# Performance work log

Hardware: AMD Instinct MI355X
Metric: run time of the kernel (lower is better)

Reference implementation:

```python
import jax, jax.numpy as jnp
import numpy as np

B, C, H, W = 8, 384, 32, 32
NUM_HEADS = 8
HEAD_DIM = C // NUM_HEADS
HIDDEN = max(32, C // 2)


def setup_inputs() -> dict:
    key = jax.random.key(0)
    ks = jax.random.split(key, 6)
    s = lambda fan_in: 1.0 / np.sqrt(fan_in)
    return {
        "x": jax.random.normal(ks[0], (B, C, H, W), dtype=jnp.float32),
        "qkv_w": jax.random.normal(ks[1], (C, 3 * C), dtype=jnp.float32) * s(C),
        "qkv_b": jnp.zeros((3 * C,), dtype=jnp.float32),
        "proj_w": jax.random.normal(ks[2], (C, C), dtype=jnp.float32) * s(C),
        "proj_b": jnp.zeros((C,), dtype=jnp.float32),
        "mlp_w1": jax.random.normal(ks[3], (2, HIDDEN), dtype=jnp.float32) * s(2),
        "mlp_b1": jnp.zeros((HIDDEN,), dtype=jnp.float32),
        "mlp_w2": jax.random.normal(ks[4], (HIDDEN, NUM_HEADS), dtype=jnp.float32) * s(HIDDEN),
        "mlp_b2": jnp.zeros((NUM_HEADS,), dtype=jnp.float32),
    }


def _relative_bias(h, w, mlp_w1, mlp_b1, mlp_w2, mlp_b2):
    ch = jnp.arange(h, dtype=jnp.float32)
    cw = jnp.arange(w, dtype=jnp.float32)
    coords = jnp.stack(jnp.meshgrid(ch, cw, indexing="ij"), axis=-1).reshape(-1, 2)  # [N,2]
    rel = coords[:, None, :] - coords[None, :, :]  # [N,N,2]
    denom = jnp.array([max(h - 1, 1), max(w - 1, 1)], dtype=jnp.float32)
    rel = rel / denom
    hidden = jax.nn.gelu(rel @ mlp_w1 + mlp_b1, approximate=False)
    bias = hidden @ mlp_w2 + mlp_b2  # [N,N,heads]
    return jnp.transpose(bias, (2, 0, 1))  # [heads,N,N]


def reference(x, qkv_w, qkv_b, proj_w, proj_b, mlp_w1, mlp_b1, mlp_w2, mlp_b2):
    b, c, h, w = x.shape
    n = h * w
    tokens = x.reshape(b, c, n).transpose(0, 2, 1)  # [B,N,C]
    qkv = (tokens @ qkv_w + qkv_b).reshape(b, n, 3, NUM_HEADS, HEAD_DIM)
    qkv = jnp.transpose(qkv, (2, 0, 3, 1, 4))  # [3,B,h,N,d]
    q, k, v = qkv[0], qkv[1], qkv[2]
    scale = HEAD_DIM ** -0.5
    attn = jnp.einsum("bhnd,bhmd->bhnm", q * scale, k)
    attn = attn + _relative_bias(h, w, mlp_w1, mlp_b1, mlp_w2, mlp_b2)[None]
    attn = jax.nn.softmax(attn, axis=-1)
    out = jnp.einsum("bhnm,bhmd->bhnd", attn, v)
    out = out.transpose(0, 2, 1, 3).reshape(b, n, c)
    out = out @ proj_w + proj_b
    return out.transpose(0, 2, 1).reshape(b, c, h, w)
```

## Files before the change

### kernel.cpp

```cpp
#include <hip/hip_runtime.h>
#include <hip/hip_bf16.h>
#include <math.h>

#define BB 8
#define CC 384
#define NT 1024
#define NHEAD 8
#define HD 48
#define HIDDEN 192
#define THREEC 1152

typedef short short8 __attribute__((ext_vector_type(8)));
typedef short short4v __attribute__((ext_vector_type(4)));
typedef float f32x4 __attribute__((ext_vector_type(4)));
typedef unsigned int uint2v __attribute__((ext_vector_type(2)));

static __device__ __forceinline__ short bf16bits(float v) {
  __hip_bfloat16 h = __float2bfloat16(v);
  return *(short*)&h;
}
static __device__ __forceinline__ unsigned pk2(float a, float b) {
  return __builtin_amdgcn_perm(__float_as_uint(b) + 0x8000u,
                               __float_as_uint(a) + 0x8000u, 0x07060302u);
}
static __device__ __forceinline__ void lds_dma16(const void* g, void* l) {
  __builtin_amdgcn_global_load_lds((const __attribute__((address_space(1))) unsigned*)g,
                                   (__attribute__((address_space(3))) unsigned*)l, 16, 0, 0);
}

__global__ __launch_bounds__(256) void k_prep(
    const float* __restrict__ x, const float* __restrict__ qkv_w,
    const float* __restrict__ proj_w,
    const float* __restrict__ w1, const float* __restrict__ b1,
    const float* __restrict__ w2, const float* __restrict__ b2,
    __hip_bfloat16* __restrict__ xt, __hip_bfloat16* __restrict__ wtq,
    __hip_bfloat16* __restrict__ wtp, float* __restrict__ tab) {
  const int bid = blockIdx.x;
  const int tid = threadIdx.x;
  if (bid >= 3648) {
    int g = (bid - 3648) * 256 + tid;
    int p = g >> 3, jc = g & 7;
    if (p >= 63 * 63) return;
    float rh = (float)(p / 63 - 31) * (1.0f / 31.0f);
    float rw = (float)(p % 63 - 31) * (1.0f / 31.0f);
    float acc[8] = {0.f, 0.f, 0.f, 0.f, 0.f, 0.f, 0.f, 0.f};
    const int j0 = jc * 24;
#pragma unroll 4
    for (int j = j0; j < j0 + 24; j++) {
      float pre = fmaf(rh, w1[j], fmaf(rw, w1[HIDDEN + j], b1[j]));
      float gl = 0.5f * pre * (1.0f + erff(pre * 0.70710678118654752f));
#pragma unroll
      for (int h = 0; h < 8; h++) acc[h] = fmaf(gl, w2[j * 8 + h], acc[h]);
    }
#pragma unroll
    for (int msk = 1; msk <= 4; msk <<= 1)
#pragma unroll
      for (int h = 0; h < 8; h++) acc[h] += __shfl_xor(acc[h], msk);
    if (jc == 0) {
#pragma unroll
      for (int h = 0; h < 8; h++)
        tab[h * 3969 + p] = (acc[h] + b2[h]) * 1.4426950408889634f;
    }
    return;
  }
  const float* src;
  __hip_bfloat16* dst;
  int R, C, r0, c0;
  if (bid < 3072) {
    int zi = bid / 384, rem = bid % 384;
    R = 384; C = 1024;
    r0 = (rem / 32) * 32; c0 = (rem % 32) * 32;
    src = x + (size_t)zi * R * C;
    dst = xt + (size_t)zi * R * C;
  } else if (bid < 3504) {
    int i = bid - 3072;
    R = 384; C = 1152;
    r0 = (i / 36) * 32; c0 = (i % 36) * 32;
    src = qkv_w; dst = wtq;
  } else {
    int i = bid - 3504;
    R = 384; C = 384;
    r0 = (i / 12) * 32; c0 = (i % 12) * 32;
    src = proj_w; dst = wtp;
  }
  __shared__ float t[32][33];
#pragma unroll
  for (int e = 0; e < 4; e++) {
    int i = tid + e * 256;
    int r = i >> 5, c = i & 31;
    t[r][c] = src[(size_t)(r0 + r) * C + c0 + c];
  }
  __syncthreads();
#pragma unroll
  for (int e = 0; e < 4; e++) {
    int i = tid + e * 256;
    int c = i >> 5, r = i & 31;
    dst[(size_t)(c0 + c) * R + r0 + r] = __float2bfloat16(t[r][c]);
  }
}

__global__ __launch_bounds__(256) void k_qkv_mfma(
    const __hip_bfloat16* __restrict__ xt,
    const __hip_bfloat16* __restrict__ wtq,
    const float* __restrict__ qkv_b,
    __hip_bfloat16* __restrict__ Qb,
    __hip_bfloat16* __restrict__ Kb,
    __hip_bfloat16* __restrict__ Vt)
{
  __shared__ __align__(16) char smem[17408];
  short* As = (short*)smem;
  short* Bs = (short*)(smem + 8192);
  float* Vf = (float*)smem;
  const int n0 = blockIdx.x * 64;
  const int m0 = blockIdx.y * 64;
  const int tid = threadIdx.x;
  const int wv = tid >> 6, lane = tid & 63, quad = lane >> 4, lq = lane & 15;
  const int lrow = lane >> 3;
  const int gsw = ((lane & 7) ^ lrow) * 8;
  const int sw0 = (quad ^ (lq & 7)) * 8;
  const int sw1 = sw0 ^ 32;
  f32x4 acc[4];
#pragma unroll
  for (int nt = 0; nt < 4; nt++) acc[nt] = (f32x4){0.f, 0.f, 0.f, 0.f};
  for (int kk = 0; kk < CC; kk += 64) {
    __syncthreads();
    for (int c = wv; c < 16; c += 4) {
      if (c < 8)
        lds_dma16((const short*)xt + (size_t)(m0 + c * 8 + lrow) * 384 + kk + gsw,
                  smem + c * 1024);
      else
        lds_dma16((const short*)wtq + (size_t)(n0 + (c - 8) * 8 + lrow) * 384 + kk + gsw,
                  smem + 8192 + (c - 8) * 1024);
    }
    __syncthreads();
    short8 a0 = *(const short8*)(As + (wv * 16 + lq) * 64 + sw0);
    short8 a1 = *(const short8*)(As + (wv * 16 + lq) * 64 + sw1);
#pragma unroll
    for (int nt = 0; nt < 4; nt++) {
      acc[nt] = __builtin_amdgcn_mfma_f32_16x16x32_bf16(
          a0, *(const short8*)(Bs + (nt * 16 + lq) * 64 + sw0), acc[nt], 0, 0, 0);
      acc[nt] = __builtin_amdgcn_mfma_f32_16x16x32_bf16(
          a1, *(const short8*)(Bs + (nt * 16 + lq) * 64 + sw1), acc[nt], 0, 0, 0);
    }
  }
  __syncthreads();
  const float qscale = 0.14433756729740643f * 1.4426950408889634f;
  const float sc = (n0 < 384) ? qscale : 1.0f;
#pragma unroll
  for (int nt = 0; nt < 4; nt++) {
    float bias = qkv_b[n0 + nt * 16 + lq];
#pragma unroll
    for (int r = 0; r < 4; r++)
      Vf[(nt * 16 + lq) * 68 + wv * 16 + quad * 4 + r] = (acc[nt][r] + bias) * sc;
  }
  __syncthreads();
  if (n0 >= 768) {
    int ch = tid & 63, grp = tid >> 6;
    int cg = n0 - 768 + ch;
    int head = cg / 48, d = cg - head * 48;
    int b = m0 >> 10;
    int n = (m0 & 1023) + grp * 16;
    const float* src = Vf + ch * 68 + grp * 16;
    short o16[16];
#pragma unroll
    for (int k = 0; k < 16; k++) o16[k] = bf16bits(src[k]);
    short* dst = (short*)Vt + ((size_t)(b * 8 + head) * 48 + d) * 1024 + n;
    *(short8*)dst = *(short8*)o16;
    *(short8*)(dst + 8) = *(short8*)(o16 + 8);
  } else {
    const int which = n0 >= 384;
    short* Out = which ? (short*)Kb : (short*)Qb;
    int n_l = tid & 63, seg = tid >> 6;
    int rr0 = (n0 - which * 384) + seg * 16;
    int head = rr0 / 48, d0 = rr0 - head * 48;
    int b = m0 >> 10;
    int n_g = (m0 & 1023) + n_l;
    const float* src = Vf + (seg * 16) * 68 + n_l;
    short o16[16];
#pragma unroll
    for (int k = 0; k < 16; k++) o16[k] = bf16bits(src[k * 68]);
    short* dst = Out + (((size_t)(b * 8 + head) << 10) + n_g) * 64 + d0;
    *(short8*)dst = *(short8*)o16;
    *(short8*)(dst + 8) = *(short8*)(o16 + 8);
    if (d0 == 0) {
      short8 z = (short8){0, 0, 0, 0, 0, 0, 0, 0};
      *(short8*)(dst + 48) = z;
      *(short8*)(dst + 56) = z;
    }
  }
}

#define K0_OFF 0
#define K1_OFF 8192
#define V0_OFF 16384
#define V1_OFF 22528
#define TR_OFF 28672
#define PS_OFF 30720
#define SMEM_SZ 39936
__global__ __launch_bounds__(256, 4) void k_flash(
    const __hip_bfloat16* __restrict__ Qb, const __hip_bfloat16* __restrict__ Kb,
    const __hip_bfloat16* __restrict__ Vt, const float* __restrict__ tab,
    __hip_bfloat16* __restrict__ ATb)
{
  __shared__ __align__(16) char smem[SMEM_SZ];
  short* Ps_l = (short*)(smem + PS_OFF);
  float* Os = (float*)smem;

  const int tid = threadIdx.x;
  const int wv = tid >> 6, lane = tid & 63, quad = lane >> 4, lq = lane & 15;
  const int bh = blockIdx.x;
  const int q0 = blockIdx.y * 64;
  const int b = bh >> 3, h = bh & 7;
  const int inr0 = q0 >> 5;

  const int nrow = q0 + wv * 16 + lq;
  const int jnr = nrow & 31;
  const int rloc = (nrow >> 5) - inr0 + 1;
  const int tbase = rloc * 63 + jnr + 31 - 4 * quad;

  short8 qf0, qf1;
  {
    const short* qp = (const short*)Qb + ((size_t)(bh << 10) + nrow) * 64;
    qf0 = *(const short8*)(qp + quad * 8);
    qf1 = *(const short8*)(qp + 32 + quad * 8);
  }
  short8 onesv;
#pragma unroll
  for (int j = 0; j < 8; j++) onesv[j] = (short)0x3F80;

  f32x4 O[4];
#pragma unroll
  for (int dt = 0; dt < 4; dt++) O[dt] = (f32x4){0.f, 0.f, 0.f, 0.f};

  const short* kgp = (const short*)Kb + ((size_t)(bh << 10)) * 64;
  const short* vgp = (const short*)Vt + (size_t)bh * 48 * 1024;
  const float* tabg = tab + h * 3969;
  const int lrow = lane >> 3;
  const int gsw = ((lane & 7) ^ lrow) * 8;
  const int sw0 = (quad ^ (lq & 7)) * 8;
  const int sw1 = sw0 ^ 32;

  for (int c = wv; c < 15; c += 4) {
    if (c < 8)
      lds_dma16(kgp + (size_t)(c * 8 + lrow) * 64 + gsw, smem + K0_OFF + c * 1024);
    else if (c < 14)
      lds_dma16(vgp + (size_t)((c - 8) * 8 + lrow) * 1024 + gsw,
                smem + V0_OFF + (c - 8) * 1024);
    else
      lds_dma16(tabg + (inr0 + 30) * 63 + lane * 4, smem + TR_OFF);
  }

  for (int it = 0; it < 16; it++) {
    const int m0 = it * 64;
    const int buf = it & 1;
    __syncthreads();
    if (it < 15) {
      const int nbuf = buf ^ 1;
      const int mn = m0 + 64;
      for (int c = wv; c < 15; c += 4) {
        if (c < 8)
          lds_dma16(kgp + (size_t)(mn + c * 8 + lrow) * 64 + gsw,
                    smem + K0_OFF + nbuf * 8192 + c * 1024);
        else if (c < 14)
          lds_dma16(vgp + (size_t)((c - 8) * 8 + lrow) * 1024 + mn + gsw,
                    smem + V0_OFF + nbuf * 6144 + (c - 8) * 1024);
        else
          lds_dma16(tabg + (inr0 + 28 - 2 * it) * 63 + lane * 4,
                    smem + TR_OFF + nbuf * 1024);
      }
    }
    const short* Kl = (const short*)(smem + K0_OFF + buf * 8192);
    const short* Vl = (const short*)(smem + V0_OFF + buf * 6144);
    const float* Tl = (const float*)(smem + TR_OFF + buf * 1024);

    float s[4][4];
#pragma unroll
    for (int nt = 0; nt < 4; nt++) {
      const float* tn = Tl + tbase - (nt >= 2 ? 63 : 0) - (nt & 1) * 16;
      f32x4 c;
      c[0] = tn[0]; c[1] = tn[-1]; c[2] = tn[-2]; c[3] = tn[-3];
      c = __builtin_amdgcn_mfma_f32_16x16x32_bf16(
          *(const short8*)(Kl + (nt * 16 + lq) * 64 + sw0), qf0, c, 0, 0, 0);
      c = __builtin_amdgcn_mfma_f32_16x16x32_bf16(
          *(const short8*)(Kl + (nt * 16 + lq) * 64 + sw1), qf1, c, 0, 0, 0);
#pragma unroll
      for (int r = 0; r < 4; r++) s[nt][r] = c[r];
    }
#pragma unroll
    for (int nt = 0; nt < 4; nt++)
#pragma unroll
      for (int r = 0; r < 4; r++) s[nt][r] = exp2f(s[nt][r]);
#pragma unroll
    for (int nt = 0; nt < 4; nt++) {
      uint2v pw;
      pw[0] = pk2(s[nt][0], s[nt][1]);
      pw[1] = pk2(s[nt][2], s[nt][3]);
      *(uint2v*)(Ps_l + (wv * 16 + lq) * 72 + nt * 16 + quad * 4) = pw;
    }
#pragma unroll
    for (int ks = 0; ks < 2; ks++) {
      short8 pf = *(const short8*)(Ps_l + (wv * 16 + lq) * 72 + ks * 32 + quad * 8);
      const int sws = ks ? sw1 : sw0;
#pragma unroll
      for (int dt = 0; dt < 3; dt++)
        O[dt] = __builtin_amdgcn_mfma_f32_16x16x32_bf16(
            *(const short8*)(Vl + (dt * 16 + lq) * 64 + sws), pf, O[dt], 0, 0, 0);
      O[3] = __builtin_amdgcn_mfma_f32_16x16x32_bf16(onesv, pf, O[3], 0, 0, 0);
    }
  }
  float inv = 1.0f / O[3][0];
  __syncthreads();
#pragma unroll
  for (int dt = 0; dt < 3; dt++)
#pragma unroll
    for (int r = 0; r < 4; r++)
      Os[(wv * 16 + lq) * 52 + dt * 16 + quad * 4 + r] = O[dt][r] * inv;
  __syncthreads();
  {
    int row = tid >> 2, cg = (tid & 3) * 12;
    const float* src = Os + row * 52 + cg;
    short outp[12];
#pragma unroll
    for (int k = 0; k < 12; k++) outp[k] = bf16bits(src[k]);
    short* dst = (short*)ATb + ((size_t)(b << 10) + q0 + row) * 384 + h * 48 + cg;
    *(short4v*)dst = *(short4v*)outp;
    *(short4v*)(dst + 4) = *(short4v*)(outp + 4);
    *(short4v*)(dst + 8) = *(short4v*)(outp + 8);
  }
}

__global__ __launch_bounds__(256) void k_proj_mfma(
    const __hip_bfloat16* __restrict__ ATb,
    const __hip_bfloat16* __restrict__ wtp,
    const float* __restrict__ pb, float* __restrict__ out) {
  __shared__ __align__(16) char smem[16384];
  short* As = (short*)smem;
  short* Bs = (short*)(smem + 8192);
  const int c0 = blockIdx.x * 64;
  const int n0 = blockIdx.y * 64;
  const int b = blockIdx.z;
  const int tid = threadIdx.x;
  const int wv = tid >> 6, lane = tid & 63, quad = lane >> 4, lq = lane & 15;
  const int lrow = lane >> 3;
  const int gsw = ((lane & 7) ^ lrow) * 8;
  const int sw0 = (quad ^ (lq & 7)) * 8;
  const int sw1 = sw0 ^ 32;
  f32x4 acc[4];
#pragma unroll
  for (int nt = 0; nt < 4; nt++) acc[nt] = (f32x4){0.f, 0.f, 0.f, 0.f};
  for (int kk = 0; kk < CC; kk += 64) {
    __syncthreads();
    for (int c = wv; c < 16; c += 4) {
      if (c < 8)
        lds_dma16((const short*)wtp + (size_t)(c0 + c * 8 + lrow) * 384 + kk + gsw,
                  smem + c * 1024);
      else
        lds_dma16((const short*)ATb + ((size_t)(b << 10) + n0 + (c - 8) * 8 + lrow) * 384 + kk + gsw,
                  smem + 8192 + (c - 8) * 1024);
    }
    __syncthreads();
    short8 a0 = *(const short8*)(As + (wv * 16 + lq) * 64 + sw0);
    short8 a1 = *(const short8*)(As + (wv * 16 + lq) * 64 + sw1);
#pragma unroll
    for (int nt = 0; nt < 4; nt++) {
      acc[nt] = __builtin_amdgcn_mfma_f32_16x16x32_bf16(
          a0, *(const short8*)(Bs + (nt * 16 + lq) * 64 + sw0), acc[nt], 0, 0, 0);
      acc[nt] = __builtin_amdgcn_mfma_f32_16x16x32_bf16(
          a1, *(const short8*)(Bs + (nt * 16 + lq) * 64 + sw1), acc[nt], 0, 0, 0);
    }
  }
#pragma unroll
  for (int nt = 0; nt < 4; nt++) {
    int n = n0 + nt * 16 + lq;
#pragma unroll
    for (int r = 0; r < 4; r++) {
      int c = c0 + wv * 16 + quad * 4 + r;
      out[((size_t)b * 384 + c) * 1024 + n] = acc[nt][r] + pb[c];
    }
  }
}

extern "C" void kernel_launch(void* const* d_in, const int* in_sizes, int n_in,
                              void* d_out, int out_size, void* d_ws, size_t ws_size,
                              hipStream_t stream) {
  const float* x = (const float*)d_in[0];
  const float* qkv_w = (const float*)d_in[1];
  const float* qkv_b = (const float*)d_in[2];
  const float* proj_w = (const float*)d_in[3];
  const float* proj_b = (const float*)d_in[4];
  const float* w1 = (const float*)d_in[5];
  const float* b1 = (const float*)d_in[6];
  const float* w2 = (const float*)d_in[7];
  const float* b2 = (const float*)d_in[8];
  float* out = (float*)d_out;

  char* w = (char*)d_ws;
  __hip_bfloat16* xt = (__hip_bfloat16*)w;   w += (size_t)8192 * 384 * 2;
  __hip_bfloat16* wtq = (__hip_bfloat16*)w;  w += (size_t)1152 * 384 * 2;
  __hip_bfloat16* wtp = (__hip_bfloat16*)w;  w += (size_t)384 * 384 * 2;
  __hip_bfloat16* Qb = (__hip_bfloat16*)w;   w += (size_t)64 * 1024 * 64 * 2;
  __hip_bfloat16* Kb = (__hip_bfloat16*)w;   w += (size_t)64 * 1024 * 64 * 2;
  __hip_bfloat16* Vt = (__hip_bfloat16*)w;   w += (size_t)64 * 48 * 1024 * 2;
  __hip_bfloat16* ATb = (__hip_bfloat16*)w;  w += (size_t)8192 * 384 * 2;
  float* tab = (float*)w;                    w += (size_t)8 * 3969 * 4 + 1024;

  k_prep<<<dim3(3773), dim3(256), 0, stream>>>(x, qkv_w, proj_w, w1, b1, w2, b2,
                                               xt, wtq, wtp, tab);
  k_qkv_mfma<<<dim3(18, 128), dim3(256), 0, stream>>>(xt, wtq, qkv_b, Qb, Kb, Vt);
  k_flash<<<dim3(64, 16), dim3(256), 0, stream>>>(Qb, Kb, Vt, tab, ATb);
  k_proj_mfma<<<dim3(6, 16, 8), dim3(256), 0, stream>>>(ATb, wtp, proj_b, out);
}
```

Baseline: 166.0 us.

## Redistribute P fragments via permlane16 swap instead of LDS round-trip

The attention-probability tile is now moved from the QK^T MFMA output layout into the PV MFMA input layout in registers, using v_permlane16_swap, instead of being written to LDS and read back. The V k-index swizzle is remapped so it matches the permuted lane order. This removes the LDS scratch buffer, which shrinks shared memory and drops a store/load pair per iteration. It also adds s_setprio around the MFMA sections so wave scheduling favours matrix issue. The risk is a mismatch in the permutation mapping, and the swap instruction only exists on newer GFX targets.

Result: no change. 166.8 us (+0.5%).

```diff
diff --git a/kernel.cpp b/kernel.cpp
--- a/kernel.cpp
+++ b/kernel.cpp
@@ -14,6 +14,7 @@
 typedef short short4v __attribute__((ext_vector_type(4)));
 typedef float f32x4 __attribute__((ext_vector_type(4)));
 typedef unsigned int uint2v __attribute__((ext_vector_type(2)));
+typedef unsigned int uint4v __attribute__((ext_vector_type(4)));
 
 static __device__ __forceinline__ short bf16bits(float v) {
   __hip_bfloat16 h = __float2bfloat16(v);
@@ -26,6 +27,9 @@
 static __device__ __forceinline__ void lds_dma16(const void* g, void* l) {
   __builtin_amdgcn_global_load_lds((const __attribute__((address_space(1))) unsigned*)g,
                                    (__attribute__((address_space(3))) unsigned*)l, 16, 0, 0);
+}
+static __device__ __forceinline__ void pl16swap(unsigned& a, unsigned& b) {
+  asm("v_permlane16_swap_b32 %0, %1" : "+v"(a), "+v"(b));
 }
 
 __global__ __launch_bounds__(256) void k_prep(
@@ -195,15 +199,13 @@
 #define V0_OFF 16384
 #define V1_OFF 22528
 #define TR_OFF 28672
-#define PS_OFF 30720
-#define SMEM_SZ 39936
+#define SMEM_SZ 30720
 __global__ __launch_bounds__(256, 4) void k_flash(
     const __hip_bfloat16* __restrict__ Qb, const __hip_bfloat16* __restrict__ Kb,
     const __hip_bfloat16* __restrict__ Vt, const float* __restrict__ tab,
     __hip_bfloat16* __restrict__ ATb)
 {
   __shared__ __align__(16) char smem[SMEM_SZ];
-  short* Ps_l = (short*)(smem + PS_OFF);
   float* Os = (float*)smem;
 
   const int tid = threadIdx.x;
@@ -239,6 +241,9 @@
   const int gsw = ((lane & 7) ^ lrow) * 8;
   const int sw0 = (quad ^ (lq & 7)) * 8;
   const int sw1 = sw0 ^ 32;
+  const int vq = ((quad & 1) << 1) | (quad >> 1);
+  const int swv0 = (vq ^ (lq & 7)) * 8;
+  const int swv1 = swv0 ^ 32;
 
   for (int c = wv; c < 15; c += 4) {
     if (c < 8)
@@ -274,6 +279,7 @@
     const float* Tl = (const float*)(smem + TR_OFF + buf * 1024);
 
     float s[4][4];
+    __builtin_amdgcn_s_setprio(1);
 #pragma unroll
     for (int nt = 0; nt < 4; nt++) {
       const float* tn = Tl + tbase - (nt >= 2 ? 63 : 0) - (nt & 1) * 16;
@@ -286,27 +292,37 @@
 #pragma unroll
       for (int r = 0; r < 4; r++) s[nt][r] = c[r];
     }
+    __builtin_amdgcn_s_setprio(0);
 #pragma unroll
     for (int nt = 0; nt < 4; nt++)
 #pragma unroll
       for (int r = 0; r < 4; r++) s[nt][r] = exp2f(s[nt][r]);
-#pragma unroll
-    for (int nt = 0; nt < 4; nt++) {
-      uint2v pw;
-      pw[0] = pk2(s[nt][0], s[nt][1]);
-      pw[1] = pk2(s[nt][2], s[nt][3]);
-      *(uint2v*)(Ps_l + (wv * 16 + lq) * 72 + nt * 16 + quad * 4) = pw;
-    }
-#pragma unroll
-    for (int ks = 0; ks < 2; ks++) {
-      short8 pf = *(const short8*)(Ps_l + (wv * 16 + lq) * 72 + ks * 32 + quad * 8);
-      const int sws = ks ? sw1 : sw0;
-#pragma unroll
-      for (int dt = 0; dt < 3; dt++)
-        O[dt] = __builtin_amdgcn_mfma_f32_16x16x32_bf16(
-            *(const short8*)(Vl + (dt * 16 + lq) * 64 + sws), pf, O[dt], 0, 0, 0);
-      O[3] = __builtin_amdgcn_mfma_f32_16x16x32_bf16(onesv, pf, O[3], 0, 0, 0);
-    }
+    uint4v p0, p1;
+    {
+      unsigned a, bb_;
+      a = pk2(s[0][0], s[0][1]); bb_ = pk2(s[1][0], s[1][1]);
+      pl16swap(a, bb_); p0[0] = a; p0[2] = bb_;
+      a = pk2(s[0][2], s[0][3]); bb_ = pk2(s[1][2], s[1][3]);
+      pl16swap(a, bb_); p0[1] = a; p0[3] = bb_;
+      a = pk2(s[2][0], s[2][1]); bb_ = pk2(s[3][0], s[3][1]);
+      pl16swap(a, bb_); p1[0] = a; p1[2] = bb_;
+      a = pk2(s[2][2], s[2][3]); bb_ = pk2(s[3][2], s[3][3]);
+      pl16swap(a, bb_); p1[1] = a; p1[3] = bb_;
+    }
+    short8 pf0 = *(short8*)&p0;
+    short8 pf1 = *(short8*)&p1;
+    __builtin_amdgcn_s_setprio(1);
+#pragma unroll
+    for (int dt = 0; dt < 3; dt++)
+      O[dt] = __builtin_amdgcn_mfma_f32_16x16x32_bf16(
+          *(const short8*)(Vl + (dt * 16 + lq) * 64 + swv0), pf0, O[dt], 0, 0, 0);
+    O[3] = __builtin_amdgcn_mfma_f32_16x16x32_bf16(onesv, pf0, O[3], 0, 0, 0);
+#pragma unroll
+    for (int dt = 0; dt < 3; dt++)
+      O[dt] = __builtin_amdgcn_mfma_f32_16x16x32_bf16(
+          *(const short8*)(Vl + (dt * 16 + lq) * 64 + swv1), pf1, O[dt], 0, 0, 0);
+    O[3] = __builtin_amdgcn_mfma_f32_16x16x32_bf16(onesv, pf1, O[3], 0, 0, 0);
+    __builtin_amdgcn_s_setprio(0);
   }
   float inv = 1.0f / O[3][0];
   __syncthreads();
```
